# Kernel optimization log

Hardware: AMD Instinct MI355X
Metric: run time of the kernel (lower is better)

## Reference

```python
import jax, jax.numpy as jnp
import numpy as np

THRESHOLD = 0.5
NEG_POS_RATIO = 3
ALPHA = 1.0
B, N_OBJ, N_PRIORS, N_CLASSES = 64, 32, 8732, 81


def xy_to_cxcy(xy):
    return jnp.concatenate([(xy[..., :2] + xy[..., 2:]) / 2.0, xy[..., 2:] - xy[..., :2]], axis=-1)


def cxcy_to_gcxgcy(cxcy, priors):
    return jnp.concatenate([
        (cxcy[..., :2] - priors[..., :2]) / (priors[..., 2:] / 10.0),
        jnp.log(cxcy[..., 2:] / priors[..., 2:]) * 5.0,
    ], axis=-1)


def jaccard(a, b):
    # a: [n,4], b: [m,4], both interpreted as (x1,y1,x2,y2) -- the original code
    # passes priors_cxcy directly (faithfully reproduced here).
    lt = jnp.maximum(a[:, None, :2], b[None, :, :2])
    rb = jnp.minimum(a[:, None, 2:], b[None, :, 2:])
    inter = jnp.prod(jnp.clip(rb - lt, 0.0, None), axis=-1)          # [n,m]
    area_a = jnp.prod(a[:, 2:] - a[:, :2], axis=-1)                  # [n]
    area_b = jnp.prod(b[:, 2:] - b[:, :2], axis=-1)                  # [m]
    return inter / (area_a[:, None] + area_b[None, :] - inter)


def _match(boxes_i, labels_i, priors_cxcy):
    # boxes_i: [n_obj,4] xy, labels_i: [n_obj] int, priors_cxcy: [n_priors,4]
    n_obj = boxes_i.shape[0]
    ov = jaccard(boxes_i, priors_cxcy)                               # [n_obj, n_priors]
    ov_for_prior = ov.max(axis=0)                                    # [n_priors]
    obj_for_prior = ov.argmax(axis=0)                                # [n_priors]
    prior_for_obj = ov.argmax(axis=1)                                # [n_obj]
    obj_for_prior = obj_for_prior.at[prior_for_obj].set(jnp.arange(n_obj))
    ov_for_prior = ov_for_prior.at[prior_for_obj].set(1.0)
    lab = labels_i[obj_for_prior]
    lab = jnp.where(ov_for_prior < THRESHOLD, 0, lab)                # background
    true_locs = cxcy_to_gcxgcy(xy_to_cxcy(boxes_i[obj_for_prior]), priors_cxcy)
    return true_locs, lab


def setup_inputs() -> dict:
    key = jax.random.key(0)
    k1, k2, k3, k4, k5, k6, k7 = jax.random.split(key, 7)
    predicted_locs = jax.random.normal(k1, (B, N_PRIORS, 4), dtype=jnp.float32)
    predicted_scores = jax.random.normal(k2, (B, N_PRIORS, N_CLASSES), dtype=jnp.float32)
    # valid gt boxes in xy form, inside [0,1]
    cxy = 0.15 + 0.7 * jax.random.uniform(k3, (B, N_OBJ, 2))
    wh = 0.05 + 0.25 * jax.random.uniform(k4, (B, N_OBJ, 2))
    boxes = jnp.clip(jnp.concatenate([cxy - wh / 2, cxy + wh / 2], axis=-1), 0.0, 1.0).astype(jnp.float32)
    labels = jax.random.randint(k5, (B, N_OBJ), 1, N_CLASSES)        # foreground classes
    # priors: cx,cy small, w,h large so that treating (cx,cy,w,h) as xy (as the
    # original code does in jaccard) still yields positive areas
    p_cxy = 0.4 * jax.random.uniform(k6, (N_PRIORS, 2))
    p_wh = 0.5 + 0.5 * jax.random.uniform(k7, (N_PRIORS, 2))
    priors_cxcy = jnp.concatenate([p_cxy, p_wh], axis=-1).astype(jnp.float32)
    return {
        "predicted_locs": predicted_locs,
        "predicted_scores": predicted_scores,
        "boxes": boxes,
        "labels": labels,
        "priors_cxcy": priors_cxcy,
    }


def multibox_loss(predicted_locs, predicted_scores, boxes, labels, priors_cxcy):
    n_priors = priors_cxcy.shape[0]
    true_locs, true_classes = jax.vmap(_match, in_axes=(0, 0, None))(boxes, labels, priors_cxcy)
    pos = true_classes != 0                                          # [B, n_priors]
    pos_f = pos.astype(predicted_locs.dtype)
    n_pos = pos.sum(axis=1)                                          # [B]
    n_pos_total = n_pos.sum().astype(jnp.float32)
    # nn.L1Loss(): mean over the 4 coords of positive priors
    loc_loss = (jnp.abs(predicted_locs - true_locs) * pos_f[..., None]).sum() / (n_pos_total * 4.0)
    # per-prior cross entropy
    logp = jax.nn.log_softmax(predicted_scores, axis=-1)             # [B,P,C]
    ce = -jnp.take_along_axis(logp, true_classes[..., None], axis=-1)[..., 0]  # [B,P]
    conf_pos = (ce * pos_f).sum()
    ce_neg = jnp.where(pos, 0.0, ce)
    ce_neg_sorted = -jnp.sort(-ce_neg, axis=1)                       # descending
    ranks = jnp.arange(n_priors)[None, :]
    hard = (ranks < (NEG_POS_RATIO * n_pos)[:, None]).astype(ce.dtype)
    conf_hard_neg = (ce_neg_sorted * hard).sum()
    conf_loss = (conf_hard_neg + conf_pos) / n_pos_total
    return conf_loss + ALPHA * loc_loss


def reference(predicted_locs, predicted_scores, boxes, labels, priors_cxcy):
    return multibox_loss(predicted_locs, predicted_scores, boxes, labels, priors_cxcy)
```

## Files before the change

kernel.cpp:

```cpp
#include <hip/hip_runtime.h>
#include <math.h>
#include <stdint.h>

#define BATCH 64
#define N_OBJ 32
#define NP 8732
#define NC 81
#define THRESH 0.5f
#define RPB 64


__device__ __forceinline__ float iou_box_prior(float x1, float y1, float x2, float y2,
                                               float areaA, float4 pr, float areaB) {
    float iw = fminf(x2, pr.z) - fmaxf(x1, pr.x); iw = fmaxf(iw, 0.f);
    float ih = fminf(y2, pr.w) - fmaxf(y1, pr.y); ih = fmaxf(ih, 0.f);
    float inter = iw * ih;
    return inter / (areaA + areaB - inter);
}

__global__ void k_match_prior(const float* __restrict__ boxes,
                              const float* __restrict__ priors,
                              float* __restrict__ ovp, int* __restrict__ objp,
                              int* __restrict__ n_pos, float* __restrict__ scal) {
    int i = blockIdx.y;
    int t = threadIdx.x;
    if (blockIdx.x == 0 && i == 0) {
        if (t < BATCH) n_pos[t] = 0;
        if (t < 3) scal[t] = 0.f;
    }
    __shared__ float bx[N_OBJ * 4];
    if (t < N_OBJ * 4) bx[t] = boxes[i * N_OBJ * 4 + t];
    __syncthreads();
    int p = blockIdx.x * blockDim.x + t;
    if (p >= NP) return;
    float4 pr = ((const float4*)priors)[p];
    float areaB = (pr.z - pr.x) * (pr.w - pr.y);
    float best = -1.0f; int bestj = 0;
    #pragma unroll
    for (int j = 0; j < N_OBJ; ++j) {
        float x1 = bx[j * 4 + 0], y1 = bx[j * 4 + 1], x2 = bx[j * 4 + 2], y2 = bx[j * 4 + 3];
        float areaA = (x2 - x1) * (y2 - y1);
        float v = iou_box_prior(x1, y1, x2, y2, areaA, pr, areaB);
        if (v > best) { best = v; bestj = j; }
    }
    ovp[i * NP + p] = best;
    objp[i * NP + p] = bestj;
}

__global__ void k_match_obj(const float* __restrict__ boxes,
                            const float* __restrict__ priors,
                            int* __restrict__ pfo) {
    int j = blockIdx.x, i = blockIdx.y;
    const float* bp = boxes + (i * N_OBJ + j) * 4;
    float x1 = bp[0], y1 = bp[1], x2 = bp[2], y2 = bp[3];
    float areaA = (x2 - x1) * (y2 - y1);
    float best = -1.f; int bestp = NP;
    for (int p = threadIdx.x; p < NP; p += blockDim.x) {
        float4 pr = ((const float4*)priors)[p];
        float areaB = (pr.z - pr.x) * (pr.w - pr.y);
        float v = iou_box_prior(x1, y1, x2, y2, areaA, pr, areaB);
        if (v > best) { best = v; bestp = p; }
    }
    __shared__ float sv[256];
    __shared__ int   si[256];
    int t = threadIdx.x;
    sv[t] = best; si[t] = bestp;
    __syncthreads();
    for (int s = 128; s > 0; s >>= 1) {
        if (t < s) {
            float v2 = sv[t + s]; int i2 = si[t + s];
            if (v2 > sv[t] || (v2 == sv[t] && i2 < si[t])) { sv[t] = v2; si[t] = i2; }
        }
        __syncthreads();
    }
    if (t == 0) pfo[i * N_OBJ + j] = si[0];
}

__global__ void k_force(const int* __restrict__ pfo,
                        float* __restrict__ ovp, int* __restrict__ objp) {
    int i = blockIdx.x * blockDim.x + threadIdx.x;
    if (i >= BATCH) return;
    for (int j = 0; j < N_OBJ; ++j) {
        int p = pfo[i * N_OBJ + j];
        objp[i * NP + p] = j;
        ovp[i * NP + p] = 1.0f;
    }
}

__global__ void __launch_bounds__(RPB)
k_ce(const float* __restrict__ scores,
     const float* __restrict__ plocs,
     const float* __restrict__ boxes,
     const int*   __restrict__ labels,
     const float* __restrict__ priors,
     const float* __restrict__ ovp,
     const int*   __restrict__ objp,
     float* __restrict__ ce_neg,
     int* __restrict__ n_pos, float* __restrict__ scal) {
    __shared__ __align__(16) float smem[RPB * NC];
    int i  = blockIdx.y;
    int p0 = blockIdx.x * RPB;
    int rows = NP - p0; if (rows > RPB) rows = RPB;
    int t = threadIdx.x;

    const float4* g4 = (const float4*)(scores + ((size_t)i * NP + p0) * NC);
    float4* s4 = (float4*)smem;
    int cnt4 = (rows * NC) >> 2;
    #pragma unroll
    for (int j = 0; j < (RPB * NC) / (4 * RPB) + 1; ++j) {
        int idx = t + j * RPB;
        if (idx < cnt4) s4[idx] = g4[idx];
    }
    __syncthreads();
    if (t >= rows) return;

    int gi  = i * NP + p0 + t;
    int   obj = objp[gi];
    float ov  = ovp[gi];
    int   lab = (ov < THRESH) ? 0 : labels[i * N_OBJ + obj];

    const float* row = smem + t * NC;
    float slab = row[lab];

    float x[NC];
    #pragma unroll
    for (int e = 0; e < NC; ++e) x[e] = row[e];

    float m0 = x[0], m1 = x[1], m2 = x[2], m3 = x[3];
    #pragma unroll
    for (int e = 4; e + 3 < NC; e += 4) {
        m0 = fmaxf(m0, x[e + 0]);
        m1 = fmaxf(m1, x[e + 1]);
        m2 = fmaxf(m2, x[e + 2]);
        m3 = fmaxf(m3, x[e + 3]);
    }
    m0 = fmaxf(m0, x[NC - 1]);
    float m = fmaxf(fmaxf(m0, m1), fmaxf(m2, m3));

    float s0 = 0.f, s1 = 0.f, s2 = 0.f, s3 = 0.f;
    #pragma unroll
    for (int e = 0; e + 3 < NC; e += 4) {
        s0 += __expf(x[e + 0] - m);
        s1 += __expf(x[e + 1] - m);
        s2 += __expf(x[e + 2] - m);
        s3 += __expf(x[e + 3] - m);
    }
    s0 += __expf(x[NC - 1] - m);
    float s = (s0 + s1) + (s2 + s3);

    float ce = m + __logf(s) - slab;

    if (lab != 0) {
        atomicAdd(&n_pos[i], 1);
        atomicAdd(&scal[0], ce);
        const float* bp = boxes + (i * N_OBJ + obj) * 4;
        float bx1 = bp[0], by1 = bp[1], bx2 = bp[2], by2 = bp[3];
        float bcx = (bx1 + bx2) * 0.5f, bcy = (by1 + by2) * 0.5f;
        float bw = bx2 - bx1, bh = by2 - by1;
        float4 pr = ((const float4*)priors)[p0 + t];
        float g0 = (bcx - pr.x) / (pr.z / 10.0f);
        float g1 = (bcy - pr.y) / (pr.w / 10.0f);
        float g2 = logf(bw / pr.z) * 5.0f;
        float g3 = logf(bh / pr.w) * 5.0f;
        const float* pl = plocs + (size_t)gi * 4;
        float ll = fabsf(pl[0] - g0) + fabsf(pl[1] - g1)
                 + fabsf(pl[2] - g2) + fabsf(pl[3] - g3);
        atomicAdd(&scal[2], ll);
        ce_neg[gi] = 0.f;
    } else {
        ce_neg[gi] = ce;
    }
}

__global__ void __launch_bounds__(256)
k_topk(const float* __restrict__ ce_neg,
       const int* __restrict__ n_pos, float* __restrict__ scal) {
    int i = blockIdx.x;
    int t = threadIdx.x;
    float x[35];
    #pragma unroll
    for (int j = 0; j < 35; ++j) {
        int p = t + j * 256;
        x[j] = (p < NP) ? ce_neg[i * NP + p] : 0.f;
    }
    int k = 3 * n_pos[i];
    if (k > NP) k = NP;
    if (k <= 0) return;

    __shared__ int   cnt_s[4];
    __shared__ float sum_s[4];
    unsigned lo = 0u, hi = 0x7F800001u;
    while (hi - lo > 1u) {
        unsigned mid = lo + ((hi - lo) >> 1);
        int c = 0;
        #pragma unroll
        for (int j = 0; j < 35; ++j) c += (__float_as_uint(x[j]) >= mid) ? 1 : 0;
        #pragma unroll
        for (int off = 32; off; off >>= 1) c += __shfl_xor(c, off);
        if ((t & 63) == 0) cnt_s[t >> 6] = c;
        __syncthreads();
        int total = cnt_s[0] + cnt_s[1] + cnt_s[2] + cnt_s[3];
        __syncthreads();
        if (total >= k) lo = mid; else hi = mid;
    }
    float vk = __uint_as_float(lo);

    float s = 0.f; int c = 0;
    #pragma unroll
    for (int j = 0; j < 35; ++j) {
        float v = x[j];
        if (v > vk) { s += v; c++; }
    }
    #pragma unroll
    for (int off = 32; off; off >>= 1) { s += __shfl_xor(s, off); c += __shfl_xor(c, off); }
    if ((t & 63) == 0) { sum_s[t >> 6] = s; cnt_s[t >> 6] = c; }
    __syncthreads();
    if (t == 0) {
        float st = sum_s[0] + sum_s[1] + sum_s[2] + sum_s[3];
        int   ct = cnt_s[0] + cnt_s[1] + cnt_s[2] + cnt_s[3];
        atomicAdd(&scal[1], st + (float)(k - ct) * vk);
    }
}

__global__ void k_final(const int* __restrict__ n_pos,
                        const float* __restrict__ scal, float* __restrict__ out) {
    int t = threadIdx.x;
    int v = (t < BATCH) ? n_pos[t] : 0;
    #pragma unroll
    for (int off = 32; off; off >>= 1) v += __shfl_xor(v, off);
    if (t == 0) {
        float nf = (float)v;
        out[0] = (scal[1] + scal[0]) / nf + scal[2] / (nf * 4.0f);
    }
}

extern "C" void kernel_launch(void* const* d_in, const int* in_sizes, int n_in,
                              void* d_out, int out_size, void* d_ws, size_t ws_size,
                              hipStream_t stream) {
    const float* plocs  = (const float*)d_in[0];
    const float* scores = (const float*)d_in[1];
    const float* boxes  = (const float*)d_in[2];
    const int*   labels = (const int*)d_in[3];
    const float* priors = (const float*)d_in[4];
    float* out = (float*)d_out;

    char* ws = (char*)d_ws;
    size_t bp = (size_t)BATCH * NP * 4;
    float* ovp    = (float*)(ws);
    int*   objp   = (int*)  (ws + bp);
    float* ce_neg = (float*)(ws + 2 * bp);
    int*   pfo    = (int*)  (ws + 3 * bp);
    int*   n_pos  = pfo + BATCH * N_OBJ;
    float* scal   = (float*)(n_pos + BATCH);

    hipLaunchKernelGGL(k_match_prior, dim3((NP + 255) / 256, BATCH), dim3(256), 0, stream,
                       boxes, priors, ovp, objp, n_pos, scal);
    hipLaunchKernelGGL(k_match_obj, dim3(N_OBJ, BATCH), dim3(256), 0, stream,
                       boxes, priors, pfo);
    hipLaunchKernelGGL(k_force, dim3(1), dim3(64), 0, stream, pfo, ovp, objp);
    hipLaunchKernelGGL(k_ce, dim3((NP + RPB - 1) / RPB, BATCH), dim3(RPB), 0, stream,
                       scores, plocs, boxes, labels, priors, ovp, objp, ce_neg, n_pos, scal);
    hipLaunchKernelGGL(k_topk, dim3(BATCH), dim3(256), 0, stream, ce_neg, n_pos, scal);
    hipLaunchKernelGGL(k_final, dim3(1), dim3(64), 0, stream, n_pos, scal, out);
}
```

Before: 196.3 us.

## Load score tiles with 256 threads and read logits straight from LDS

The cross-entropy kernel now launches 256 threads per block. All of them cooperatively copy the 64-row score tile into shared memory, then only the first 64 threads compute per-prior softmax. The per-thread 81-element register copy of the row is removed, and max/sum are computed by reading shared memory directly. This is meant to raise memory-level parallelism on the dominant score read and cut register pressure. The cost is idle waves after the load and extra LDS reads.

Result: faster. 189.9 us (-3.3%).

```diff
diff --git a/kernel.cpp b/kernel.cpp
--- a/kernel.cpp
+++ b/kernel.cpp
@@ -87,7 +87,7 @@
     }
 }
 
-__global__ void __launch_bounds__(RPB)
+__global__ void __launch_bounds__(256)
 k_ce(const float* __restrict__ scores,
      const float* __restrict__ plocs,
      const float* __restrict__ boxes,
@@ -107,8 +107,8 @@
     float4* s4 = (float4*)smem;
     int cnt4 = (rows * NC) >> 2;
     #pragma unroll
-    for (int j = 0; j < (RPB * NC) / (4 * RPB) + 1; ++j) {
-        int idx = t + j * RPB;
+    for (int j = 0; j < 6; ++j) {
+        int idx = t + j * 256;
         if (idx < cnt4) s4[idx] = g4[idx];
     }
     __syncthreads();
@@ -122,30 +122,26 @@
     const float* row = smem + t * NC;
     float slab = row[lab];
 
-    float x[NC];
-    #pragma unroll
-    for (int e = 0; e < NC; ++e) x[e] = row[e];
-
-    float m0 = x[0], m1 = x[1], m2 = x[2], m3 = x[3];
+    float m0 = row[0], m1 = row[1], m2 = row[2], m3 = row[3];
     #pragma unroll
     for (int e = 4; e + 3 < NC; e += 4) {
-        m0 = fmaxf(m0, x[e + 0]);
-        m1 = fmaxf(m1, x[e + 1]);
-        m2 = fmaxf(m2, x[e + 2]);
-        m3 = fmaxf(m3, x[e + 3]);
-    }
-    m0 = fmaxf(m0, x[NC - 1]);
+        m0 = fmaxf(m0, row[e + 0]);
+        m1 = fmaxf(m1, row[e + 1]);
+        m2 = fmaxf(m2, row[e + 2]);
+        m3 = fmaxf(m3, row[e + 3]);
+    }
+    m0 = fmaxf(m0, row[NC - 1]);
     float m = fmaxf(fmaxf(m0, m1), fmaxf(m2, m3));
 
     float s0 = 0.f, s1 = 0.f, s2 = 0.f, s3 = 0.f;
     #pragma unroll
     for (int e = 0; e + 3 < NC; e += 4) {
-        s0 += __expf(x[e + 0] - m);
-        s1 += __expf(x[e + 1] - m);
-        s2 += __expf(x[e + 2] - m);
-        s3 += __expf(x[e + 3] - m);
-    }
-    s0 += __expf(x[NC - 1] - m);
+        s0 += __expf(row[e + 0] - m);
+        s1 += __expf(row[e + 1] - m);
+        s2 += __expf(row[e + 2] - m);
+        s3 += __expf(row[e + 3] - m);
+    }
+    s0 += __expf(row[NC - 1] - m);
     float s = (s0 + s1) + (s2 + s3);
 
     float ce = m + __logf(s) - slab;
@@ -258,7 +254,7 @@
     hipLaunchKernelGGL(k_match_obj, dim3(N_OBJ, BATCH), dim3(256), 0, stream,
                        boxes, priors, pfo);
     hipLaunchKernelGGL(k_force, dim3(1), dim3(64), 0, stream, pfo, ovp, objp);
-    hipLaunchKernelGGL(k_ce, dim3((NP + RPB - 1) / RPB, BATCH), dim3(RPB), 0, stream,
+    hipLaunchKernelGGL(k_ce, dim3((NP + RPB - 1) / RPB, BATCH), dim3(256), 0, stream,
                        scores, plocs, boxes, labels, priors, ovp, objp, ce_neg, n_pos, scal);
     hipLaunchKernelGGL(k_topk, dim3(BATCH), dim3(256), 0, stream, ce_neg, n_pos, scal);
     hipLaunchKernelGGL(k_final, dim3(1), dim3(64), 0, stream, n_pos, scal, out);
```
